# Performance work log

Measured on AMD Instinct MI355X. Metric: run time of the kernel, lower is better.

## Reference

```python
import jax, jax.numpy as jnp
import numpy as np

VOCAB = 32000
WDIM = 768      # bert-base hidden size, per self.w_dim
H = 512         # lstm_hidden
NUM_CAT = 5
START = 3       # l2ind['SOS']
END = 4         # l2ind['EOS']
T = 2048
NEG = -10000.0


def _lstm_dir(x, Wih, Whh, bih, bhh, reverse):
    # x: [T, WDIM]; torch LSTM gate order: i, f, g, o
    z_in = x @ Wih.T + bih + bhh  # [T, 4H] precompute input projection
    def step(carry, zt):
        h, c = carry
        z = zt + h @ Whh.T
        i, f, g, o = jnp.split(z, 4)
        c = jax.nn.sigmoid(f) * c + jax.nn.sigmoid(i) * jnp.tanh(g)
        h = jax.nn.sigmoid(o) * jnp.tanh(c)
        return (h, c), h
    init = (jnp.zeros((H,), x.dtype), jnp.zeros((H,), x.dtype))
    _, hs = jax.lax.scan(step, init, z_in, reverse=reverse)
    return hs  # [T, H], aligned with input order


def setup_inputs():
    key = jax.random.key(0)
    ks = jax.random.split(key, 13)
    s = 0.05
    sent = jax.random.randint(ks[0], (T,), 0, VOCAB)
    emb = jax.random.normal(ks[1], (VOCAB, WDIM), jnp.float32) * 0.02
    Wih_f = jax.random.normal(ks[2], (4 * H, WDIM), jnp.float32) * s
    Whh_f = jax.random.normal(ks[3], (4 * H, H), jnp.float32) * s
    bih_f = jax.random.normal(ks[4], (4 * H,), jnp.float32) * s
    bhh_f = jax.random.normal(ks[5], (4 * H,), jnp.float32) * s
    Wih_b = jax.random.normal(ks[6], (4 * H, WDIM), jnp.float32) * s
    Whh_b = jax.random.normal(ks[7], (4 * H, H), jnp.float32) * s
    bih_b = jax.random.normal(ks[8], (4 * H,), jnp.float32) * s
    bhh_b = jax.random.normal(ks[9], (4 * H,), jnp.float32) * s
    fc_w = jax.random.normal(ks[10], (NUM_CAT, 2 * H), jnp.float32) * s
    fc_b = jax.random.normal(ks[11], (NUM_CAT,), jnp.float32) * s
    transitions = jax.random.normal(ks[12], (NUM_CAT, NUM_CAT), jnp.float32)
    transitions = transitions.at[START, :].set(NEG).at[:, END].set(NEG)
    return {"sent": sent, "emb": emb,
            "Wih_f": Wih_f, "Whh_f": Whh_f, "bih_f": bih_f, "bhh_f": bhh_f,
            "Wih_b": Wih_b, "Whh_b": Whh_b, "bih_b": bih_b, "bhh_b": bhh_b,
            "fc_w": fc_w, "fc_b": fc_b, "transitions": transitions}


def reference(sent, emb, Wih_f, Whh_f, bih_f, bhh_f, Wih_b, Whh_b, bih_b, bhh_b, fc_w, fc_b, transitions):
    # _get_scores: embedding -> BiLSTM -> fc
    x = emb[sent]                                   # [T, WDIM]
    h_f = _lstm_dir(x, Wih_f, Whh_f, bih_f, bhh_f, reverse=False)
    h_b = _lstm_dir(x, Wih_b, Whh_b, bih_b, bhh_b, reverse=True)
    out = jnp.concatenate([h_f, h_b], axis=-1)      # [T, 2H]
    feats = out @ fc_w.T + fc_b                     # [T, NUM_CAT]

    # _viterbi_decode: transitions[i, j] = score of moving from tag j to tag i
    init = feats[0] + transitions[:, START]         # [NUM_CAT]
    def vstep(layer, feat_t):
        # scores[i, j] = feat_t[i] + transitions[i, j] + layer[j]
        scores = feat_t[:, None] + transitions + layer[None, :]
        return jnp.max(scores, axis=1), jnp.argmax(scores, axis=1)
    layer, parents = jax.lax.scan(vstep, init, feats[1:])  # parents: [T-1, NUM_CAT]

    final = layer + transitions[END]
    idx0 = jnp.argmax(final)
    path_score = jnp.max(final)

    # backtrack (parents[0] of the original loop is all-START and gets popped)
    def btrack(idx, p):
        nxt = p[idx]
        return nxt, nxt
    _, idxs = jax.lax.scan(btrack, idx0, parents, reverse=True)  # [T-1]
    path = jnp.concatenate([idxs, idx0[None]])      # [T]
    return path, path_score
```

## Files before the change

### kernel.cpp

```cpp
#include <hip/hip_runtime.h>

#define TT 2048
#define WD 768
#define HH 512
#define G4 2048
#define NC 5
#define SENT 0xFFFFFFFFu

typedef float f4 __attribute__((ext_vector_type(4)));
typedef unsigned int u4 __attribute__((ext_vector_type(4)));

__global__ __launch_bounds__(256) void zin_gemm(
    const int* __restrict__ sent, const float* __restrict__ emb,
    const float* __restrict__ Wih_f, const float* __restrict__ bih_f, const float* __restrict__ bhh_f,
    const float* __restrict__ Wih_b, const float* __restrict__ bih_b, const float* __restrict__ bhh_b,
    float* __restrict__ zin_f, float* __restrict__ zin_b)
{
    const int dirn = blockIdx.z;
    const float* Wih = dirn ? Wih_b : Wih_f;
    const float* bih = dirn ? bih_b : bih_f;
    const float* bhh = dirn ? bhh_b : bhh_f;
    float* zin = dirn ? zin_b : zin_f;

    __shared__ float As[16][128];
    __shared__ float Bs[16][128];

    const int tid = threadIdx.x;
    const int t0 = blockIdx.y * 128;
    const int g0 = blockIdx.x * 128;
    const int tm = tid >> 4, tn = tid & 15;

    float acc[8][8];
#pragma unroll
    for (int a = 0; a < 8; a++)
#pragma unroll
        for (int b = 0; b < 8; b++) acc[a][b] = 0.f;

    for (int kt = 0; kt < 48; ++kt) {
        const int k0 = kt * 16;
#pragma unroll
        for (int u = 0; u < 2; ++u) {
            const int s = tid * 2 + u;
            const int m = s >> 2, kq = s & 3;
            const int rowA = sent[t0 + m];
            float4 av = *(const float4*)(emb + (size_t)rowA * WD + k0 + kq * 4);
            As[kq * 4 + 0][m] = av.x; As[kq * 4 + 1][m] = av.y;
            As[kq * 4 + 2][m] = av.z; As[kq * 4 + 3][m] = av.w;
            float4 bv = *(const float4*)(Wih + (size_t)(g0 + m) * WD + k0 + kq * 4);
            Bs[kq * 4 + 0][m] = bv.x; Bs[kq * 4 + 1][m] = bv.y;
            Bs[kq * 4 + 2][m] = bv.z; Bs[kq * 4 + 3][m] = bv.w;
        }
        __syncthreads();
#pragma unroll
        for (int kk = 0; kk < 16; ++kk) {
            float4 a0 = *(const float4*)&As[kk][tm * 8];
            float4 a1 = *(const float4*)&As[kk][tm * 8 + 4];
            float4 b0 = *(const float4*)&Bs[kk][tn * 8];
            float4 b1 = *(const float4*)&Bs[kk][tn * 8 + 4];
            float av8[8] = {a0.x, a0.y, a0.z, a0.w, a1.x, a1.y, a1.z, a1.w};
            float bv8[8] = {b0.x, b0.y, b0.z, b0.w, b1.x, b1.y, b1.z, b1.w};
#pragma unroll
            for (int a = 0; a < 8; a++)
#pragma unroll
                for (int b = 0; b < 8; b++) acc[a][b] += av8[a] * bv8[b];
        }
        __syncthreads();
    }
    float bias[8];
#pragma unroll
    for (int b = 0; b < 8; b++) { int g = g0 + tn * 8 + b; bias[b] = bih[g] + bhh[g]; }
#pragma unroll
    for (int a = 0; a < 8; a++) {
        const int t = t0 + tm * 8 + a;
        float* op = zin + (size_t)t * G4 + g0 + tn * 8;
        float4 o0 = {acc[a][0] + bias[0], acc[a][1] + bias[1], acc[a][2] + bias[2], acc[a][3] + bias[3]};
        float4 o1 = {acc[a][4] + bias[4], acc[a][5] + bias[5], acc[a][6] + bias[6], acc[a][7] + bias[7]};
        *(float4*)op = o0; *(float4*)(op + 4) = o1;
    }
}

__global__ __launch_bounds__(256, 1) void lstm_rec(
    const float* __restrict__ zin_f, const float* __restrict__ zin_b,
    const float* __restrict__ Whh_f, const float* __restrict__ Whh_b,
    unsigned int* __restrict__ hw_f, unsigned int* __restrict__ hw_b)
{
    const int bid = blockIdx.x;
    const int d = bid >> 5;
    const int k = bid & 31;
    const float* zin = d ? zin_b : zin_f;
    const float* Whh = d ? Whh_b : Whh_f;
    unsigned int* hw = d ? hw_b : hw_f;

    const int tid = threadIdx.x;
    const int q = tid >> 6;
    const int r = tid & 63;
    const int gate = r >> 4, jj = r & 15;
    const int grow = gate * HH + k * 16 + jj;

    const f4* wp = (const f4*)(Whh + (size_t)grow * HH + q * 128);
    f4 w[32];
#pragma unroll
    for (int i = 0; i < 32; ++i) w[i] = wp[i];
#pragma unroll
    for (int i = 0; i < 32; ++i)
        asm volatile("" : "+a"(w[i]));

    __shared__ float hs[HH];
    __shared__ float zb[256];

    float c = 0.f;
    const int l = tid;
    const int g = l >> 4, j = l & 15;
    const int n16 = k * 16 + j;

    for (int it = 0; it < TT; ++it) {
        const int t = d ? (TT - 1 - it) : it;

        float z = 0.f;
        if (tid < 64) z = zin[(size_t)t * G4 + g * HH + n16];

        if (it > 0 && tid < 64) {
            const int tp = d ? (t + 1) : (t - 1);
            const unsigned int* pa = hw + (size_t)tp * HH + l * 8;
            u4 a0, a1;
            for (;;) {
                asm volatile(
                    "global_load_dwordx4 %0, %2, off sc0 sc1\n\t"
                    "global_load_dwordx4 %1, %2, off offset:16 sc0 sc1\n\t"
                    "s_waitcnt vmcnt(0)"
                    : "=v"(a0), "=v"(a1) : "v"(pa) : "memory");
                if (a0.x != SENT && a0.y != SENT && a0.z != SENT && a0.w != SENT &&
                    a1.x != SENT && a1.y != SENT && a1.z != SENT && a1.w != SENT) break;
            }
            u4* hd = (u4*)(hs + l * 8);
            hd[0] = a0; hd[1] = a1;
        }
        __syncthreads();

#pragma unroll
        for (int i = 0; i < 32; ++i) asm volatile("" : "+a"(w[i]));

        float part = 0.f;
        if (it > 0) {
            const f4* hv = ((const f4*)hs) + (q << 5);
#pragma unroll
            for (int i = 0; i < 32; ++i) {
                f4 h4 = hv[i];
                part += w[i].x * h4.x + w[i].y * h4.y + w[i].z * h4.z + w[i].w * h4.w;
            }
        }
        zb[tid] = part;
        __syncthreads();

        if (tid < 64) {
            float s = zb[l] + zb[64 + l] + zb[128 + l] + zb[192 + l];
            const float pre = z + s;
            float act;
            if (g == 2) act = tanhf(pre);
            else        act = 1.f / (1.f + expf(-pre));
            const float gi = __shfl(act, j);
            const float gf = __shfl(act, j + 16);
            const float gg = __shfl(act, j + 32);
            const float go = __shfl(act, j + 48);
            if (l < 16) {
                c = gf * c + gi * gg;
                const float hval = go * tanhf(c);
                __hip_atomic_store(&hw[(size_t)t * HH + k * 16 + l],
                                   __float_as_uint(hval),
                                   __ATOMIC_RELAXED, __HIP_MEMORY_SCOPE_AGENT);
            }
        }
    }
}

__global__ void feats_kernel(const float* __restrict__ h_f, const float* __restrict__ h_b,
                             const float* __restrict__ fc_w, const float* __restrict__ fc_b,
                             float* __restrict__ feats)
{
    const int t = blockIdx.x;
    const int l = threadIdx.x;
    float acc[NC] = {0.f, 0.f, 0.f, 0.f, 0.f};
    for (int m = 0; m < 16; ++m) {
        const int cg = l + m * 64;
        const float hv = (cg < HH) ? h_f[(size_t)t * HH + cg]
                                   : h_b[(size_t)t * HH + cg - HH];
#pragma unroll
        for (int i = 0; i < NC; i++) acc[i] += hv * fc_w[i * (2 * HH) + cg];
    }
#pragma unroll
    for (int i = 0; i < NC; i++) {
#pragma unroll
        for (int off = 32; off; off >>= 1) acc[i] += __shfl_xor(acc[i], off);
    }
    if (l == 0) {
#pragma unroll
        for (int i = 0; i < NC; i++) feats[(size_t)t * NC + i] = acc[i] + fc_b[i];
    }
}

__global__ void viterbi_kernel(const float* __restrict__ feats,
                               const float* __restrict__ trans,
                               float* __restrict__ out)
{
    __shared__ float fs[TT * NC];
    __shared__ int par[TT];
    __shared__ float pathv[TT];
    const int tid = threadIdx.x;
    for (int i = tid; i < TT * NC; i += 64) fs[i] = feats[i];
    float tr[25];
#pragma unroll
    for (int i = 0; i < 25; i++) tr[i] = trans[i];
    __syncthreads();

    float layer[NC];
#pragma unroll
    for (int i = 0; i < NC; i++) layer[i] = fs[i] + tr[i * 5 + 3];

    for (int s = 0; s < TT - 1; ++s) {
        const float* ft = &fs[(s + 1) * NC];
        float nl[NC]; int pk = 0;
#pragma unroll
        for (int i = 0; i < NC; i++) {
            float best = tr[i * 5 + 0] + layer[0]; int bj = 0;
#pragma unroll
            for (int jj = 1; jj < NC; jj++) {
                const float v = tr[i * 5 + jj] + layer[jj];
                if (v > best) { best = v; bj = jj; }
            }
            nl[i] = ft[i] + best;
            pk |= bj << (3 * i);
        }
#pragma unroll
        for (int i = 0; i < NC; i++) layer[i] = nl[i];
        if (tid == 0) par[s] = pk;
    }
    float best = layer[0] + tr[20]; int idx0 = 0;
#pragma unroll
    for (int jj = 1; jj < NC; jj++) {
        const float v = layer[jj] + tr[20 + jj];
        if (v > best) { best = v; idx0 = jj; }
    }
    __syncthreads();
    if (tid == 0) {
        pathv[TT - 1] = (float)idx0;
        int idx = idx0;
        for (int s = TT - 2; s >= 0; --s) {
            idx = (par[s] >> (3 * idx)) & 7;
            pathv[s] = (float)idx;
        }
        out[TT] = best;
    }
    __syncthreads();
    for (int i = tid; i < TT; i += 64) out[i] = pathv[i];
}

extern "C" void kernel_launch(void* const* d_in, const int* in_sizes, int n_in,
                              void* d_out, int out_size, void* d_ws, size_t ws_size,
                              hipStream_t stream) {
    const int*   sent   = (const int*)d_in[0];
    const float* emb    = (const float*)d_in[1];
    const float* Wih_f  = (const float*)d_in[2];
    const float* Whh_f  = (const float*)d_in[3];
    const float* bih_f  = (const float*)d_in[4];
    const float* bhh_f  = (const float*)d_in[5];
    const float* Wih_b  = (const float*)d_in[6];
    const float* Whh_b  = (const float*)d_in[7];
    const float* bih_b  = (const float*)d_in[8];
    const float* bhh_b  = (const float*)d_in[9];
    const float* fc_w   = (const float*)d_in[10];
    const float* fc_b   = (const float*)d_in[11];
    const float* trans  = (const float*)d_in[12];
    float* out = (float*)d_out;

    char* ws = (char*)d_ws;
    float* zin_f = (float*)ws;
    float* zin_b = (float*)(ws + (size_t)16777216);
    unsigned int* hw_f = (unsigned int*)(ws + (size_t)33554432);
    unsigned int* hw_b = (unsigned int*)(ws + (size_t)37748736);
    float* feats = (float*)(ws + (size_t)41943040);

    hipMemsetAsync(hw_f, 0xFF, (size_t)8388608, stream);

    dim3 gg(G4 / 128, TT / 128, 2);
    zin_gemm<<<gg, 256, 0, stream>>>(sent, emb, Wih_f, bih_f, bhh_f,
                                     Wih_b, bih_b, bhh_b, zin_f, zin_b);

    lstm_rec<<<64, 256, 0, stream>>>(zin_f, zin_b, Whh_f, Whh_b, hw_f, hw_b);

    feats_kernel<<<TT, 64, 0, stream>>>((const float*)hw_f, (const float*)hw_b,
                                        fc_w, fc_b, feats);

    viterbi_kernel<<<1, 64, 0, stream>>>(feats, trans, out);
}
```

Before: 4.771 ms.

## Fuse input-projection GEMM into LSTM recurrence kernel with per-tile readiness counters

Merges the zin GEMM and the LSTM recurrence into one launch. Blocks 0-63 run the recurrence and blocks 64+ compute GEMM tiles, ordered so each direction's earliest timesteps are produced first. GEMM blocks bump a per-(direction, time-tile) counter after storing, and recurrence blocks spin on it before reading that tile's zin. The goal is to hide GEMM time behind the serial recurrence and drop a kernel boundary. It relies on all 576 blocks being co-resident or scheduled in order to avoid deadlock, and it adds polling traffic.

```diff
diff --git a/kernel.cpp b/kernel.cpp
--- a/kernel.cpp
+++ b/kernel.cpp
@@ -10,80 +10,92 @@
 typedef float f4 __attribute__((ext_vector_type(4)));
 typedef unsigned int u4 __attribute__((ext_vector_type(4)));
 
-__global__ __launch_bounds__(256) void zin_gemm(
+__global__ __launch_bounds__(256, 1) void fused_main(
     const int* __restrict__ sent, const float* __restrict__ emb,
     const float* __restrict__ Wih_f, const float* __restrict__ bih_f, const float* __restrict__ bhh_f,
     const float* __restrict__ Wih_b, const float* __restrict__ bih_b, const float* __restrict__ bhh_b,
-    float* __restrict__ zin_f, float* __restrict__ zin_b)
+    const float* __restrict__ Whh_f, const float* __restrict__ Whh_b,
+    float* __restrict__ zin_f, float* __restrict__ zin_b,
+    unsigned int* __restrict__ hw_f, unsigned int* __restrict__ hw_b,
+    unsigned int* __restrict__ zcnt)
 {
-    const int dirn = blockIdx.z;
-    const float* Wih = dirn ? Wih_b : Wih_f;
-    const float* bih = dirn ? bih_b : bih_f;
-    const float* bhh = dirn ? bhh_b : bhh_f;
-    float* zin = dirn ? zin_b : zin_f;
-
     __shared__ float As[16][128];
     __shared__ float Bs[16][128];
+    __shared__ float hs[HH];
+    __shared__ float zb[256];
 
     const int tid = threadIdx.x;
-    const int t0 = blockIdx.y * 128;
-    const int g0 = blockIdx.x * 128;
-    const int tm = tid >> 4, tn = tid & 15;
-
-    float acc[8][8];
-#pragma unroll
-    for (int a = 0; a < 8; a++)
-#pragma unroll
-        for (int b = 0; b < 8; b++) acc[a][b] = 0.f;
-
-    for (int kt = 0; kt < 48; ++kt) {
-        const int k0 = kt * 16;
-#pragma unroll
-        for (int u = 0; u < 2; ++u) {
-            const int s = tid * 2 + u;
-            const int m = s >> 2, kq = s & 3;
-            const int rowA = sent[t0 + m];
-            float4 av = *(const float4*)(emb + (size_t)rowA * WD + k0 + kq * 4);
-            As[kq * 4 + 0][m] = av.x; As[kq * 4 + 1][m] = av.y;
-            As[kq * 4 + 2][m] = av.z; As[kq * 4 + 3][m] = av.w;
-            float4 bv = *(const float4*)(Wih + (size_t)(g0 + m) * WD + k0 + kq * 4);
-            Bs[kq * 4 + 0][m] = bv.x; Bs[kq * 4 + 1][m] = bv.y;
-            Bs[kq * 4 + 2][m] = bv.z; Bs[kq * 4 + 3][m] = bv.w;
+
+    if (blockIdx.x >= 64) {
+        const int lin  = blockIdx.x - 64;
+        const int pair = lin >> 5;
+        const int sub  = lin & 31;
+        const int dirn = sub & 1;
+        const int gx   = sub >> 1;
+        const int ty   = dirn ? (15 - pair) : pair;
+
+        const float* Wih = dirn ? Wih_b : Wih_f;
+        const float* bih = dirn ? bih_b : bih_f;
+        const float* bhh = dirn ? bhh_b : bhh_f;
+        float* zin = dirn ? zin_b : zin_f;
+
+        const int t0 = ty * 128;
+        const int g0 = gx * 128;
+        const int tm = tid >> 4, tn = tid & 15;
+
+        float acc[8][8];
+#pragma unroll
+        for (int a = 0; a < 8; a++)
+#pragma unroll
+            for (int b = 0; b < 8; b++) acc[a][b] = 0.f;
+
+        for (int kt = 0; kt < 48; ++kt) {
+            const int k0 = kt * 16;
+#pragma unroll
+            for (int u = 0; u < 2; ++u) {
+                const int s = tid * 2 + u;
+                const int m = s >> 2, kq = s & 3;
+                const int rowA = sent[t0 + m];
+                float4 av = *(const float4*)(emb + (size_t)rowA * WD + k0 + kq * 4);
+                As[kq * 4 + 0][m] = av.x; As[kq * 4 + 1][m] = av.y;
+                As[kq * 4 + 2][m] = av.z; As[kq * 4 + 3][m] = av.w;
+                float4 bv = *(const float4*)(Wih + (size_t)(g0 + m) * WD + k0 + kq * 4);
+                Bs[kq * 4 + 0][m] = bv.x; Bs[kq * 4 + 1][m] = bv.y;
+                Bs[kq * 4 + 2][m] = bv.z; Bs[kq * 4 + 3][m] = bv.w;
+            }
+            __syncthreads();
+#pragma unroll
+            for (int kk = 0; kk < 16; ++kk) {
+                float4 a0 = *(const float4*)&As[kk][tm * 8];
+                float4 a1 = *(const float4*)&As[kk][tm * 8 + 4];
+                float4 b0 = *(const float4*)&Bs[kk][tn * 8];
+                float4 b1 = *(const float4*)&Bs[kk][tn * 8 + 4];
+                float av8[8] = {a0.x, a0.y, a0.z, a0.w, a1.x, a1.y, a1.z, a1.w};
+                float bv8[8] = {b0.x, b0.y, b0.z, b0.w, b1.x, b1.y, b1.z, b1.w};
+#pragma unroll
+                for (int a = 0; a < 8; a++)
+#pragma unroll
+                    for (int b = 0; b < 8; b++) acc[a][b] += av8[a] * bv8[b];
+            }
+            __syncthreads();
+        }
+        float bias[8];
+#pragma unroll
+        for (int b = 0; b < 8; b++) { int g = g0 + tn * 8 + b; bias[b] = bih[g] + bhh[g]; }
+#pragma unroll
+        for (int a = 0; a < 8; a++) {
+            const int t = t0 + tm * 8 + a;
+            float* op = zin + (size_t)t * G4 + g0 + tn * 8;
+            f4 o0 = {acc[a][0] + bias[0], acc[a][1] + bias[1], acc[a][2] + bias[2], acc[a][3] + bias[3]};
+            f4 o1 = {acc[a][4] + bias[4], acc[a][5] + bias[5], acc[a][6] + bias[6], acc[a][7] + bias[7]};
+            asm volatile("global_store_dwordx4 %0, %1, off sc1" :: "v"(op), "v"(o0) : "memory");
+            asm volatile("global_store_dwordx4 %0, %1, off sc1" :: "v"(op + 4), "v"(o1) : "memory");
         }
         __syncthreads();
-#pragma unroll
-        for (int kk = 0; kk < 16; ++kk) {
-            float4 a0 = *(const float4*)&As[kk][tm * 8];
-            float4 a1 = *(const float4*)&As[kk][tm * 8 + 4];
-            float4 b0 = *(const float4*)&Bs[kk][tn * 8];
-            float4 b1 = *(const float4*)&Bs[kk][tn * 8 + 4];
-            float av8[8] = {a0.x, a0.y, a0.z, a0.w, a1.x, a1.y, a1.z, a1.w};
-            float bv8[8] = {b0.x, b0.y, b0.z, b0.w, b1.x, b1.y, b1.z, b1.w};
-#pragma unroll
-            for (int a = 0; a < 8; a++)
-#pragma unroll
-                for (int b = 0; b < 8; b++) acc[a][b] += av8[a] * bv8[b];
-        }
-        __syncthreads();
-    }
-    float bias[8];
-#pragma unroll
-    for (int b = 0; b < 8; b++) { int g = g0 + tn * 8 + b; bias[b] = bih[g] + bhh[g]; }
-#pragma unroll
-    for (int a = 0; a < 8; a++) {
-        const int t = t0 + tm * 8 + a;
-        float* op = zin + (size_t)t * G4 + g0 + tn * 8;
-        float4 o0 = {acc[a][0] + bias[0], acc[a][1] + bias[1], acc[a][2] + bias[2], acc[a][3] + bias[3]};
-        float4 o1 = {acc[a][4] + bias[4], acc[a][5] + bias[5], acc[a][6] + bias[6], acc[a][7] + bias[7]};
-        *(float4*)op = o0; *(float4*)(op + 4) = o1;
-    }
-}
-
-__global__ __launch_bounds__(256, 1) void lstm_rec(
-    const float* __restrict__ zin_f, const float* __restrict__ zin_b,
-    const float* __restrict__ Whh_f, const float* __restrict__ Whh_b,
-    unsigned int* __restrict__ hw_f, unsigned int* __restrict__ hw_b)
-{
+        if (tid == 0) atomicAdd(&zcnt[dirn * 16 + ty], 1u);
+        return;
+    }
+
     const int bid = blockIdx.x;
     const int d = bid >> 5;
     const int k = bid & 31;
@@ -91,7 +103,6 @@
     const float* Whh = d ? Whh_b : Whh_f;
     unsigned int* hw = d ? hw_b : hw_f;
 
-    const int tid = threadIdx.x;
     const int q = tid >> 6;
     const int r = tid & 63;
     const int gate = r >> 4, jj = r & 15;
@@ -105,19 +116,31 @@
     for (int i = 0; i < 32; ++i)
         asm volatile("" : "+a"(w[i]));
 
-    __shared__ float hs[HH];
-    __shared__ float zb[256];
-
     float c = 0.f;
     const int l = tid;
     const int g = l >> 4, j = l & 15;
     const int n16 = k * 16 + j;
 
+    int readyty = -1;
+
     for (int it = 0; it < TT; ++it) {
         const int t = d ? (TT - 1 - it) : it;
 
         float z = 0.f;
-        if (tid < 64) z = zin[(size_t)t * G4 + g * HH + n16];
+        if (tid < 64) {
+            const int tyc = t >> 7;
+            if (tyc != readyty) {
+                const unsigned int* cp = zcnt + d * 16 + tyc;
+                unsigned int cv;
+                do {
+                    asm volatile("global_load_dword %0, %1, off sc0 sc1\n\t"
+                                 "s_waitcnt vmcnt(0)"
+                                 : "=v"(cv) : "v"(cp) : "memory");
+                } while (cv < 16u);
+                readyty = tyc;
+            }
+            z = zin[(size_t)t * G4 + g * HH + n16];
+        }
 
         if (it > 0 && tid < 64) {
             const int tp = d ? (t + 1) : (t - 1);
@@ -278,14 +301,16 @@
     unsigned int* hw_f = (unsigned int*)(ws + (size_t)33554432);
     unsigned int* hw_b = (unsigned int*)(ws + (size_t)37748736);
     float* feats = (float*)(ws + (size_t)41943040);
+    unsigned int* zcnt = (unsigned int*)(ws + (size_t)42008576);
 
     hipMemsetAsync(hw_f, 0xFF, (size_t)8388608, stream);
-
-    dim3 gg(G4 / 128, TT / 128, 2);
-    zin_gemm<<<gg, 256, 0, stream>>>(sent, emb, Wih_f, bih_f, bhh_f,
-                                     Wih_b, bih_b, bhh_b, zin_f, zin_b);
-
-    lstm_rec<<<64, 256, 0, stream>>>(zin_f, zin_b, Whh_f, Whh_b, hw_f, hw_b);
+    hipMemsetAsync(zcnt, 0, (size_t)128, stream);
+
+    fused_main<<<576, 256, 0, stream>>>(sent, emb,
+                                        Wih_f, bih_f, bhh_f,
+                                        Wih_b, bih_b, bhh_b,
+                                        Whh_f, Whh_b,
+                                        zin_f, zin_b, hw_f, hw_b, zcnt);
 
     feats_kernel<<<TT, 64, 0, stream>>>((const float*)hw_f, (const float*)hw_b,
                                         fc_w, fc_b, feats);
```

New measurement: 4.781 ms. About the same (+0.2%).
